# Performance work log

Measured on AMD Instinct MI355X. Metric: run time of the kernel, lower is better.

Reference implementation:

```python
import jax, jax.numpy as jnp
import numpy as np

G = 1.0      # gravitational constant from G_Nbody(graph, 1.0, eps=1e-10)
EPS = 1e-10  # softening epsilon
N_BODIES = 4096


def setup_inputs() -> dict:
    key = jax.random.key(0)
    kx, = jax.random.split(key, 1)
    x = jax.random.normal(kx, (N_BODIES, 4), dtype=jnp.float32)  # [N, 2q + 2p]
    m = jnp.ones((N_BODIES, 1), dtype=jnp.float32)               # node masses g.ndata['m']
    return {"x": x, "m": m}


def _hamiltonian(x, m):
    # x: [N, 4] = (q, p); m: [N, 1]
    q, p = jnp.split(x, 2, axis=-1)
    # Kinetic: faithful to create_kin's T[0,0,:].sum() -> all |p_j|^2 divided by 2*m_0
    K = jnp.sum(p * p) / (2.0 * m[0, 0])
    # Potential: all-pairs, Us[j, i] = G * m_i * m_j / (|q_j - q_i| + eps)
    diff = q[:, None, :] - q[None, :, :]          # [N, N, 2], diff[j, i] = q_j - q_i
    sq = jnp.sum(diff * diff, axis=-1)            # [N, N]
    n = x.shape[0]
    eye = jnp.eye(n, dtype=bool)
    dist = jnp.sqrt(jnp.where(eye, 1.0, sq))      # safe sqrt on diagonal (r=0 self-pair)
    mu = G * (m * m.T)                            # [N, N]
    # diagonal self-pair contributes constant mu/eps (zero q-gradient), as in original
    Us = jnp.where(eye, mu / EPS, mu / (dist + EPS))
    idx = jnp.arange(n)
    keep = idx[None, :] <= idx[:, None] + 1       # torch.tril(Us, diagonal=1)
    U = jnp.sum(jnp.where(keep, Us, 0.0))
    return K + U


def reference(x, m):
    # forward(t, x): dH/dx, then return cat(dH/dp, -dH/dq) (symplectic vector field)
    dHdx = jax.grad(_hamiltonian)(x, m)           # [N, 4]
    dHdq, dHdp = jnp.split(dHdx, 2, axis=-1)
    return jnp.concatenate((dHdp, -dHdq), axis=-1)
```

## Files before the change

### kernel.cpp

```cpp
#include <hip/hip_runtime.h>

#define NB 4096
#define TPB 1024
#define WPB (TPB / 64)
#define NBLK (NB / WPB)
#define NPAIR (NB / 2)
#define NT (NPAIR / 64)

__global__ __launch_bounds__(TPB) void nbody_wave(
    const float* __restrict__ x, const float* __restrict__ m,
    float4* __restrict__ out)
{
    __shared__ float4 qp[NPAIR];
    __shared__ float2 mp[NPAIR];

    const int tid = threadIdx.x;

    #pragma unroll
    for (int t = 0; t < NPAIR / TPB; ++t) {
        const int j = t * TPB + tid;
        const float4 a = ((const float4*)x)[2 * j];
        const float4 b = ((const float4*)x)[2 * j + 1];
        qp[j] = make_float4(a.x, a.y, b.x, b.y);
        mp[j] = ((const float2*)m)[j];
    }
    __syncthreads();

    const int wave = tid >> 6;
    const int lane = tid & 63;
    const int k = blockIdx.x * WPB + wave;

    const float4 xk = ((const float4*)x)[k];
    const float qx = xk.x, qy = xk.y;
    float ax = 0.f, ay = 0.f;

    #pragma unroll 8
    for (int t = 0; t < NT; ++t) {
        const int p = t * 64 + lane;
        const float4 q = qp[p];
        const float2 mm = mp[p];
        {
            const float dx = qx - q.x;
            const float dy = qy - q.y;
            float sq = fmaf(dx, dx, dy * dy);
            sq = fmaxf(sq, 1e-12f);
            const float r = __builtin_amdgcn_rsqf(sq);
            const float w = r * r * r * mm.x;
            ax = fmaf(dx, w, ax);
            ay = fmaf(dy, w, ay);
        }
        {
            const float dx = qx - q.z;
            const float dy = qy - q.w;
            float sq = fmaf(dx, dx, dy * dy);
            sq = fmaxf(sq, 1e-12f);
            const float r = __builtin_amdgcn_rsqf(sq);
            const float w = r * r * r * mm.y;
            ax = fmaf(dx, w, ax);
            ay = fmaf(dy, w, ay);
        }
    }

    int nbi = -1;
    if (lane == 0 && k > 0) nbi = k - 1;
    else if (lane == 1 && k < NB - 1) nbi = k + 1;
    if (nbi >= 0) {
        const float4 q = qp[nbi >> 1];
        const float2 mm = mp[nbi >> 1];
        const float sx = (nbi & 1) ? q.z : q.x;
        const float sy = (nbi & 1) ? q.w : q.y;
        const float sm = (nbi & 1) ? mm.y : mm.x;
        const float dx = qx - sx;
        const float dy = qy - sy;
        const float sq = fmaf(dx, dx, dy * dy);
        const float r = __builtin_amdgcn_rsqf(sq);
        const float w = r * r * r * sm;
        ax = fmaf(dx, w, ax);
        ay = fmaf(dy, w, ay);
    }

    #pragma unroll
    for (int off = 32; off > 0; off >>= 1) {
        ax += __shfl_xor(ax, off);
        ay += __shfl_xor(ay, off);
    }

    if (lane == 0) {
        const float m0inv = 1.0f / m[0];
        out[k] = make_float4(xk.z * m0inv, xk.w * m0inv, ax * m[k], ay * m[k]);
    }
}

extern "C" void kernel_launch(void* const* d_in, const int* in_sizes, int n_in,
                              void* d_out, int out_size, void* d_ws, size_t ws_size,
                              hipStream_t stream) {
    const float* x = (const float*)d_in[0];
    const float* m = (const float*)d_in[1];
    nbody_wave<<<dim3(NBLK), dim3(TPB), 0, stream>>>(x, m, (float4*)d_out);
}
```

Before: 12.50 us.

## Split each body's interaction sum across two waves and fold softening into FMA

New measurement: 12.54 us. About the same (+0.4%).

```diff
diff --git a/kernel.cpp b/kernel.cpp
--- a/kernel.cpp
+++ b/kernel.cpp
@@ -2,17 +2,20 @@
 
 #define NB 4096
 #define TPB 1024
-#define WPB (TPB / 64)
-#define NBLK (NB / WPB)
+#define WPB 16
+#define BPB 8
+#define NBLK (NB / BPB)
 #define NPAIR (NB / 2)
-#define NT (NPAIR / 64)
+#define HALF (NPAIR / 2)
+#define NT (HALF / 64)
 
-__global__ __launch_bounds__(TPB) void nbody_wave(
+__global__ __launch_bounds__(TPB) void nbody_wave2(
     const float* __restrict__ x, const float* __restrict__ m,
     float4* __restrict__ out)
 {
     __shared__ float4 qp[NPAIR];
     __shared__ float2 mp[NPAIR];
+    __shared__ float2 red[WPB];
 
     const int tid = threadIdx.x;
 
@@ -28,22 +31,24 @@
 
     const int wave = tid >> 6;
     const int lane = tid & 63;
-    const int k = blockIdx.x * WPB + wave;
+    const int b    = wave >> 1;
+    const int h    = wave & 1;
+    const int k    = blockIdx.x * BPB + b;
 
     const float4 xk = ((const float4*)x)[k];
     const float qx = xk.x, qy = xk.y;
     float ax = 0.f, ay = 0.f;
 
+    const int base = h * HALF;
     #pragma unroll 8
     for (int t = 0; t < NT; ++t) {
-        const int p = t * 64 + lane;
+        const int p = base + t * 64 + lane;
         const float4 q = qp[p];
         const float2 mm = mp[p];
         {
             const float dx = qx - q.x;
             const float dy = qy - q.y;
-            float sq = fmaf(dx, dx, dy * dy);
-            sq = fmaxf(sq, 1e-12f);
+            const float sq = fmaf(dx, dx, fmaf(dy, dy, 1e-20f));
             const float r = __builtin_amdgcn_rsqf(sq);
             const float w = r * r * r * mm.x;
             ax = fmaf(dx, w, ax);
@@ -52,8 +57,7 @@
         {
             const float dx = qx - q.z;
             const float dy = qy - q.w;
-            float sq = fmaf(dx, dx, dy * dy);
-            sq = fmaxf(sq, 1e-12f);
+            const float sq = fmaf(dx, dx, fmaf(dy, dy, 1e-20f));
             const float r = __builtin_amdgcn_rsqf(sq);
             const float w = r * r * r * mm.y;
             ax = fmaf(dx, w, ax);
@@ -61,22 +65,24 @@
         }
     }
 
-    int nbi = -1;
-    if (lane == 0 && k > 0) nbi = k - 1;
-    else if (lane == 1 && k < NB - 1) nbi = k + 1;
-    if (nbi >= 0) {
-        const float4 q = qp[nbi >> 1];
-        const float2 mm = mp[nbi >> 1];
-        const float sx = (nbi & 1) ? q.z : q.x;
-        const float sy = (nbi & 1) ? q.w : q.y;
-        const float sm = (nbi & 1) ? mm.y : mm.x;
-        const float dx = qx - sx;
-        const float dy = qy - sy;
-        const float sq = fmaf(dx, dx, dy * dy);
-        const float r = __builtin_amdgcn_rsqf(sq);
-        const float w = r * r * r * sm;
-        ax = fmaf(dx, w, ax);
-        ay = fmaf(dy, w, ay);
+    if (h == 0) {
+        int nbi = -1;
+        if (lane == 0 && k > 0) nbi = k - 1;
+        else if (lane == 1 && k < NB - 1) nbi = k + 1;
+        if (nbi >= 0) {
+            const float4 q = qp[nbi >> 1];
+            const float2 mm = mp[nbi >> 1];
+            const float sx = (nbi & 1) ? q.z : q.x;
+            const float sy = (nbi & 1) ? q.w : q.y;
+            const float sm = (nbi & 1) ? mm.y : mm.x;
+            const float dx = qx - sx;
+            const float dy = qy - sy;
+            const float sq = fmaf(dx, dx, dy * dy);
+            const float r = __builtin_amdgcn_rsqf(sq);
+            const float w = r * r * r * sm;
+            ax = fmaf(dx, w, ax);
+            ay = fmaf(dy, w, ay);
+        }
     }
 
     #pragma unroll
@@ -85,9 +91,16 @@
         ay += __shfl_xor(ay, off);
     }
 
-    if (lane == 0) {
+    if (lane == 0) red[wave] = make_float2(ax, ay);
+    __syncthreads();
+
+    if (h == 0 && lane == 0) {
+        const float2 r0 = red[wave];
+        const float2 r1 = red[wave + 1];
+        const float sx = r0.x + r1.x;
+        const float sy = r0.y + r1.y;
         const float m0inv = 1.0f / m[0];
-        out[k] = make_float4(xk.z * m0inv, xk.w * m0inv, ax * m[k], ay * m[k]);
+        out[k] = make_float4(xk.z * m0inv, xk.w * m0inv, sx * m[k], sy * m[k]);
     }
 }
 
@@ -96,5 +109,5 @@
                               hipStream_t stream) {
     const float* x = (const float*)d_in[0];
     const float* m = (const float*)d_in[1];
-    nbody_wave<<<dim3(NBLK), dim3(TPB), 0, stream>>>(x, m, (float4*)d_out);
+    nbody_wave2<<<dim3(NBLK), dim3(TPB), 0, stream>>>(x, m, (float4*)d_out);
 }
```
